# Optimization experiments

Hardware: AMD Instinct MI355X
Metric: run time of the kernel (lower is better)

Reference implementation:

```python
import jax, jax.numpy as jnp
import numpy as np

B, L, H, E, R = 2, 512, 768, 512, 32768
H2 = H // 2


def setup_inputs() -> dict:
    key = jax.random.key(0)
    ks = jax.random.split(key, 16)
    s = 0.02
    inp = {
        "hidden_states": jax.random.normal(ks[0], (B, L, H), dtype=jnp.float32),
        "ent_start": jax.random.randint(ks[1], (B, E), 0, L, dtype=jnp.int32),
        "ent_label": jax.random.randint(ks[2], (B, E), 0, 3, dtype=jnp.int32),
        "rel_head": jax.random.randint(ks[3], (B, R), 0, E, dtype=jnp.int32),
        "rel_tail": jax.random.randint(ks[4], (B, R), 0, E, dtype=jnp.int32),
        "rel_label": jax.random.randint(ks[5], (B, R), 0, 2, dtype=jnp.int32),
        "entity_emb": jax.random.normal(ks[6], (3, H), dtype=jnp.float32) * s,
        "head_W1": jax.random.normal(ks[7], (2 * H, H), dtype=jnp.float32) * s,
        "head_b1": jnp.zeros((H,), dtype=jnp.float32),
        "head_W2": jax.random.normal(ks[8], (H, H2), dtype=jnp.float32) * s,
        "head_b2": jnp.zeros((H2,), dtype=jnp.float32),
        "tail_W1": jax.random.normal(ks[9], (2 * H, H), dtype=jnp.float32) * s,
        "tail_b1": jnp.zeros((H,), dtype=jnp.float32),
        "tail_W2": jax.random.normal(ks[10], (H, H2), dtype=jnp.float32) * s,
        "tail_b2": jnp.zeros((H2,), dtype=jnp.float32),
        "bil_W": jax.random.normal(ks[11], (2, H2, H2), dtype=jnp.float32) * s,
        "lin_W": jax.random.normal(ks[12], (2 * H2, 2), dtype=jnp.float32) * s,
        "lin_b": jnp.zeros((2,), dtype=jnp.float32),
    }
    return inp


def _mlp(x, W1, b1, W2, b2):
    # Linear -> ReLU -> (dropout=identity) -> Linear -> ReLU -> (dropout=identity)
    h = jax.nn.relu(jnp.einsum("brd,dh->brh", x, W1) + b1)
    return jax.nn.relu(jnp.einsum("brh,hk->brk", h, W2) + b2)


def reference(hidden_states, ent_start, ent_label, rel_head, rel_tail, rel_label,
              entity_emb, head_W1, head_b1, head_W2, head_b2,
              tail_W1, tail_b1, tail_W2, tail_b2, bil_W, lin_W, lin_b):
    # Gather entity start token index and label for each relation endpoint
    h_idx = jnp.take_along_axis(ent_start, rel_head, axis=1)  # [B,R]
    t_idx = jnp.take_along_axis(ent_start, rel_tail, axis=1)
    h_lab = jnp.take_along_axis(ent_label, rel_head, axis=1)
    t_lab = jnp.take_along_axis(ent_label, rel_tail, axis=1)

    # Gather hidden states at entity start positions: [B,R,H]
    h_tok = jnp.take_along_axis(hidden_states, h_idx[..., None], axis=1)
    t_tok = jnp.take_along_axis(hidden_states, t_idx[..., None], axis=1)

    head_repr = jnp.concatenate([h_tok, entity_emb[h_lab]], axis=-1)  # [B,R,2H]
    tail_repr = jnp.concatenate([t_tok, entity_emb[t_lab]], axis=-1)

    heads = _mlp(head_repr, head_W1, head_b1, head_W2, head_b2)  # [B,R,H2]
    tails = _mlp(tail_repr, tail_W1, tail_b1, tail_W2, tail_b2)

    # BiaffineAttention: bilinear(x1,x2) + linear(cat(x1,x2))
    bil = jnp.einsum("brd,ode,bre->bro", heads, bil_W, tails)  # [B,R,2]
    lin = jnp.einsum("brc,co->bro", jnp.concatenate([heads, tails], axis=-1), lin_W) + lin_b
    logits = bil + lin  # [B,R,2]

    # Per-doc mean cross-entropy, summed over docs (matches loss accumulation)
    logp = jax.nn.log_softmax(logits, axis=-1)
    ce = -jnp.take_along_axis(logp, rel_label[..., None], axis=-1)[..., 0]  # [B,R]
    loss = ce.mean(axis=-1).sum()

    return loss, logits.reshape(B * R, 2)
```

## Files before the change

kernel.cpp:

```cpp
#include <hip/hip_runtime.h>
#include <math.h>

#define BB 2
#define LL 512
#define HH 768
#define EE 512
#define RR 32768
#define H2 384
#define MM 1024

typedef __attribute__((ext_vector_type(8))) short     bf16x8;
typedef __attribute__((ext_vector_type(4))) float     f32x4;
typedef __attribute__((ext_vector_type(8))) unsigned short u16x8;

#define BUFE (64 * 136)

__device__ __forceinline__ unsigned short f2bf(float f) {
    unsigned int u = __float_as_uint(f);
    u = (u + 0x7FFFu + ((u >> 16) & 1u)) >> 16;
    return (unsigned short)u;
}

__device__ __forceinline__ void wtrans(const float* __restrict__ src,
                                       unsigned short* __restrict__ dst,
                                       int K, int N, int tile, unsigned short* T)
{
    const int t = threadIdx.x;
    const int tn = N >> 5;
    const int n0 = (tile % tn) * 32;
    const int k0 = (tile / tn) * 32;
    const int r  = t >> 3;
    const int c4 = (t & 7) * 4;
    const float4 g = *(const float4*)(src + (size_t)(k0 + r) * N + n0 + c4);
    T[(c4 + 0) * 40 + r] = f2bf(g.x);
    T[(c4 + 1) * 40 + r] = f2bf(g.y);
    T[(c4 + 2) * 40 + r] = f2bf(g.z);
    T[(c4 + 3) * 40 + r] = f2bf(g.w);
    __syncthreads();
    const int n  = t >> 3;
    const int k4 = (t & 7) * 4;
    *(ushort4*)(dst + (size_t)(n0 + n) * K + k0 + k4) = *(ushort4*)&T[n * 40 + k4];
}

__global__ __launch_bounds__(256) void prep(
    const float* __restrict__ hW1, const float* __restrict__ tW1,
    unsigned short* __restrict__ W1ht, unsigned short* __restrict__ W1tt,
    const float* __restrict__ hidden, const int* __restrict__ ent_start,
    const float* __restrict__ emb,
    const float* __restrict__ hb1, const float* __restrict__ tb1,
    unsigned short* __restrict__ Hbf, float* __restrict__ embc,
    float* __restrict__ hlin, float* __restrict__ tlin, float* __restrict__ out)
{
    __shared__ unsigned short T[32 * 40];
    __shared__ float red[4][192];
    const int bid = blockIdx.x;
    const int t = threadIdx.x;

    if (bid == 2200) {
        const float4 z = {0.f, 0.f, 0.f, 0.f};
        ((float4*)hlin)[t] = z; ((float4*)hlin)[256 + t] = z;
        ((float4*)tlin)[t] = z; ((float4*)tlin)[256 + t] = z;
        if (t == 0) out[0] = 0.f;
        return;
    }

    if (bid >= 2176) {
        const int eb = bid - 2176;
        const int tc = t & 63;
        const int kg = t >> 6;
        const int n = eb * 64 + tc;
        const float* W = (n < 768) ? hW1 : tW1;
        const int cc = (n < 768) ? n : n - 768;
        float a0 = 0.f, a1 = 0.f, a2 = 0.f;
        const int kbeg = kg * 192;
        #pragma unroll 8
        for (int k = kbeg; k < kbeg + 192; ++k) {
            const float w = W[(size_t)(768 + k) * 768 + cc];
            a0 += emb[k] * w;
            a1 += emb[768 + k] * w;
            a2 += emb[1536 + k] * w;
        }
        red[kg][0 * 64 + tc] = a0;
        red[kg][1 * 64 + tc] = a1;
        red[kg][2 * 64 + tc] = a2;
        __syncthreads();
        if (kg == 0) {
            const float b = (n < 768) ? hb1[n] : tb1[n - 768];
            #pragma unroll
            for (int l = 0; l < 3; ++l) {
                embc[l * 1536 + n] = b + red[0][l * 64 + tc] + red[1][l * 64 + tc]
                                       + red[2][l * 64 + tc] + red[3][l * 64 + tc];
            }
        }
        return;
    }

    if (bid >= 1152) {
        const int m = bid - 1152;
        if (t >= 96) return;
        const int b = m >> 9;
        const int idx = ent_start[m];
        const float4* s = (const float4*)(hidden + (size_t)(b * LL + idx) * HH);
        const float4 v0 = s[2 * t];
        const float4 v1 = s[2 * t + 1];
        u16x8 o;
        o[0] = f2bf(v0.x); o[1] = f2bf(v0.y); o[2] = f2bf(v0.z); o[3] = f2bf(v0.w);
        o[4] = f2bf(v1.x); o[5] = f2bf(v1.y); o[6] = f2bf(v1.z); o[7] = f2bf(v1.w);
        *(u16x8*)(Hbf + (size_t)m * 768 + 8 * t) = o;
        return;
    }

    if (bid < 576) wtrans(hW1, W1ht, 768, 768, bid, T);
    else           wtrans(tW1, W1tt, 768, 768, bid - 576, T);
}

template<bool RELU, bool BIAS, bool EB, bool WF32, bool WBF16, bool O2, bool LIN>
__device__ __forceinline__ void gemm_body(
    int tile, int nx,
    const unsigned short* __restrict__ A, int lda, int aoff1,
    const unsigned short* __restrict__ Bt0, const unsigned short* __restrict__ Bt1,
    int ldb, int bt_mrow, int Nh,
    const float* __restrict__ bias0, const float* __restrict__ bias1,
    const float* __restrict__ embc, const int* __restrict__ labels,
    const float* __restrict__ linW, float* __restrict__ hlin, float* __restrict__ tlin,
    int K, float* __restrict__ Cf, unsigned short* __restrict__ Cb, int ldc,
    unsigned short* As, unsigned short* Bs)
{
    const int tid = threadIdx.x;
    const int n0 = (tile % nx) * 64;
    const int m0 = (tile / nx) * 64;
    const int hf = (n0 >= Nh) ? 1 : 0;
    const unsigned short* Bt = hf ? Bt1 : Bt0;
    const int nc0 = n0 - (hf ? Nh : 0);
    const int aoff = hf ? aoff1 : 0;

    const int sr = tid >> 2;
    const int sk = (tid & 3) * 32;

    const unsigned short* Ap = A + (size_t)(m0 + sr) * lda + aoff + sk;
    const unsigned short* Bp = Bt + (size_t)((m0 >> 9) * bt_mrow + nc0 + sr) * ldb + sk;

    const int lane = tid & 63;
    const int wave = tid >> 6;
    const int wm = (wave & 1) * 32;
    const int wn = (wave >> 1) * 32;
    const int l15 = lane & 15;
    const int quad = lane >> 4;

    f32x4 acc00 = {}, acc01 = {}, acc10 = {}, acc11 = {};

    u16x8 av0 = *(const u16x8*)(Ap);      u16x8 av1 = *(const u16x8*)(Ap + 8);
    u16x8 av2 = *(const u16x8*)(Ap + 16); u16x8 av3 = *(const u16x8*)(Ap + 24);
    u16x8 bv0 = *(const u16x8*)(Bp);      u16x8 bv1 = *(const u16x8*)(Bp + 8);
    u16x8 bv2 = *(const u16x8*)(Bp + 16); u16x8 bv3 = *(const u16x8*)(Bp + 24);
    const int swo = sr * 136 + sk;
    *(u16x8*)&As[swo] = av0;      *(u16x8*)&As[swo + 8] = av1;
    *(u16x8*)&As[swo + 16] = av2; *(u16x8*)&As[swo + 24] = av3;
    *(u16x8*)&Bs[swo] = bv0;      *(u16x8*)&Bs[swo + 8] = bv1;
    *(u16x8*)&Bs[swo + 16] = bv2; *(u16x8*)&Bs[swo + 24] = bv3;

    const int NT = K >> 7;
    const int aro = quad * 8;
    int cur = 0;
    for (int it = 0; it < NT; ++it) {
        if (it + 1 < NT) {
            const int ko = (it + 1) * 128;
            av0 = *(const u16x8*)(Ap + ko);      av1 = *(const u16x8*)(Ap + ko + 8);
            av2 = *(const u16x8*)(Ap + ko + 16); av3 = *(const u16x8*)(Ap + ko + 24);
            bv0 = *(const u16x8*)(Bp + ko);      bv1 = *(const u16x8*)(Bp + ko + 8);
            bv2 = *(const u16x8*)(Bp + ko + 16); bv3 = *(const u16x8*)(Bp + ko + 24);
        }
        asm volatile("s_waitcnt lgkmcnt(0)" ::: "memory");
        __builtin_amdgcn_s_barrier();
        __builtin_amdgcn_sched_barrier(0);
        const unsigned short* Ac = As + cur * BUFE;
        const unsigned short* Bc = Bs + cur * BUFE;
        #pragma unroll
        for (int s = 0; s < 4; ++s) {
            const int ks = s * 32 + aro;
            const bf16x8 fa0 = *(const bf16x8*)&Ac[(wm + l15) * 136 + ks];
            const bf16x8 fa1 = *(const bf16x8*)&Ac[(wm + 16 + l15) * 136 + ks];
            const bf16x8 fb0 = *(const bf16x8*)&Bc[(wn + l15) * 136 + ks];
            const bf16x8 fb1 = *(const bf16x8*)&Bc[(wn + 16 + l15) * 136 + ks];
            acc00 = __builtin_amdgcn_mfma_f32_16x16x32_bf16(fa0, fb0, acc00, 0, 0, 0);
            acc01 = __builtin_amdgcn_mfma_f32_16x16x32_bf16(fa0, fb1, acc01, 0, 0, 0);
            acc10 = __builtin_amdgcn_mfma_f32_16x16x32_bf16(fa1, fb0, acc10, 0, 0, 0);
            acc11 = __builtin_amdgcn_mfma_f32_16x16x32_bf16(fa1, fb1, acc11, 0, 0, 0);
        }
        if (it + 1 < NT) {
            unsigned short* Aw = As + (cur ^ 1) * BUFE;
            unsigned short* Bw = Bs + (cur ^ 1) * BUFE;
            *(u16x8*)&Aw[swo] = av0;      *(u16x8*)&Aw[swo + 8] = av1;
            *(u16x8*)&Aw[swo + 16] = av2; *(u16x8*)&Aw[swo + 24] = av3;
            *(u16x8*)&Bw[swo] = bv0;      *(u16x8*)&Bw[swo + 8] = bv1;
            *(u16x8*)&Bw[swo + 16] = bv2; *(u16x8*)&Bw[swo + 24] = bv3;
        }
        cur ^= 1;
    }

    float bias_v0 = 0.f, bias_v1 = 0.f;
    if (BIAS) {
        const float* bb = hf ? bias1 : bias0;
        bias_v0 = bb[nc0 + wn + l15];
        bias_v1 = bb[nc0 + wn + 16 + l15];
    }
    const int col0 = n0 + wn + l15;
    const int col1 = col0 + 16;
    int colw0 = col0, colw1 = col1;
    if (O2) {
        colw0 = 2 * (nc0 + wn + l15) + hf;
        colw1 = 2 * (nc0 + wn + 16 + l15) + hf;
    }
    float2 lw0 = {0.f, 0.f}, lw1 = {0.f, 0.f};
    float* lout = nullptr;
    if (LIN) {
        lw0 = ((const float2*)linW)[col0];
        lw1 = ((const float2*)linW)[col1];
        lout = hf ? tlin : hlin;
    }
    const f32x4 accs[2][2] = {{acc00, acc01}, {acc10, acc11}};
    #pragma unroll
    for (int mi = 0; mi < 2; ++mi) {
        #pragma unroll
        for (int r = 0; r < 4; ++r) {
            const int row = m0 + wm + mi * 16 + quad * 4 + r;
            float v0 = accs[mi][0][r];
            float v1 = accs[mi][1][r];
            if (BIAS) { v0 += bias_v0; v1 += bias_v1; }
            if (EB) {
                const int lab = labels[row];
                v0 += embc[lab * 1536 + col0];
                v1 += embc[lab * 1536 + col1];
            }
            if (RELU) { v0 = fmaxf(v0, 0.f); v1 = fmaxf(v1, 0.f); }
            if (WF32) {
                Cf[(size_t)row * ldc + colw0] = v0;
                Cf[(size_t)row * ldc + colw1] = v1;
            }
            if (WBF16) {
                Cb[(size_t)row * ldc + colw0] = f2bf(v0);
                Cb[(size_t)row * ldc + colw1] = f2bf(v1);
            }
            if (LIN) {
                float s0 = v0 * lw0.x + v1 * lw1.x;
                float s1 = v0 * lw0.y + v1 * lw1.y;
                #pragma unroll
                for (int o = 8; o >= 1; o >>= 1) {
                    s0 += __shfl_xor(s0, o, 64);
                    s1 += __shfl_xor(s1, o, 64);
                }
                if (l15 == 0) {
                    atomicAdd(&lout[2 * row],     s0);
                    atomicAdd(&lout[2 * row + 1], s1);
                }
            }
        }
    }
}

template<bool RELU, bool BIAS, bool EB, bool WF32, bool WBF16, bool O2, bool LIN>
__global__ __launch_bounds__(256) void gemm_mfma(
    const unsigned short* __restrict__ A, int lda, int aoff1,
    const unsigned short* __restrict__ Bt0, const unsigned short* __restrict__ Bt1,
    int ldb, int bt_mrow, int Nh,
    const float* __restrict__ bias0, const float* __restrict__ bias1,
    const float* __restrict__ embc, const int* __restrict__ labels,
    const float* __restrict__ linW, float* __restrict__ hlin, float* __restrict__ tlin,
    int K, float* __restrict__ Cf, unsigned short* __restrict__ Cb, int ldc)
{
    __shared__ __align__(16) unsigned short As[2 * BUFE];
    __shared__ __align__(16) unsigned short Bs[2 * BUFE];
    gemm_body<RELU, BIAS, EB, WF32, WBF16, O2, LIN>(
        blockIdx.y * gridDim.x + blockIdx.x, gridDim.x,
        A, lda, aoff1, Bt0, Bt1, ldb, bt_mrow, Nh,
        bias0, bias1, embc, labels, linW, hlin, tlin,
        K, Cf, Cb, ldc, As, Bs);
}

__global__ __launch_bounds__(256) void gemm1_plus(
    const unsigned short* __restrict__ Hbf,
    const unsigned short* __restrict__ W1ht, const unsigned short* __restrict__ W1tt,
    const float* __restrict__ embc, const int* __restrict__ ent_label,
    unsigned short* __restrict__ Y1bf,
    const float* __restrict__ hW2, const float* __restrict__ tW2,
    const float* __restrict__ bilW,
    unsigned short* __restrict__ W2ht, unsigned short* __restrict__ W2tt,
    unsigned short* __restrict__ bW0t, unsigned short* __restrict__ bW1t)
{
    __shared__ __align__(16) unsigned short As[2 * BUFE];
    __shared__ __align__(16) unsigned short Bs[2 * BUFE];
    const int bid = blockIdx.x;
    if (bid >= 384) {
        const int task = bid - 384;
        if (task < 288)      wtrans(hW2, W2ht, 768, 384, task, As);
        else if (task < 576) wtrans(tW2, W2tt, 768, 384, task - 288, As);
        else if (task < 720) wtrans(bilW, bW0t, 384, 384, task - 576, As);
        else                 wtrans(bilW + 384 * 384, bW1t, 384, 384, task - 720, As);
        return;
    }
    gemm_body<true, false, true, false, true, false, false>(
        bid, 24, Hbf, 768, 0, W1ht, W1tt, 768, 0, 768,
        nullptr, nullptr, embc, ent_label, nullptr, nullptr, nullptr,
        768, nullptr, Y1bf, 1536, As, Bs);
}

__global__ __launch_bounds__(256) void rel_gather(
    const float* __restrict__ Stab,
    const float* __restrict__ hlin, const float* __restrict__ tlin,
    const float* __restrict__ lin_b,
    const int* __restrict__ rel_head, const int* __restrict__ rel_tail,
    const int* __restrict__ rel_label,
    float* __restrict__ out)
{
    const int tid = threadIdx.x;
    const int i = blockIdx.x * 256 + tid;
    const int b = i >> 15;
    const int h = rel_head[i];
    const int t = rel_tail[i];
    const int lab = rel_label[i];
    const int mh = (b << 9) + h;
    const int mt = (b << 9) + t;

    const float2 hl = ((const float2*)hlin)[mh];
    const float2 tl = ((const float2*)tlin)[mt];
    const float2 zz = *(const float2*)(Stab + (size_t)mh * 1024 + 2 * t);
    const float z0 = zz.x + hl.x + tl.x + lin_b[0];
    const float z1 = zz.y + hl.y + tl.y + lin_b[1];
    out[1 + 2 * (size_t)i] = z0;
    out[2 + 2 * (size_t)i] = z1;

    const float mx = fmaxf(z0, z1);
    const float mn = fminf(z0, z1);
    const float lse = mx + log1pf(expf(mn - mx));
    float ce = lse - (lab ? z1 : z0);

    #pragma unroll
    for (int o = 32; o >= 1; o >>= 1) ce += __shfl_xor(ce, o, 64);
    __shared__ float wsum[4];
    if ((tid & 63) == 0) wsum[tid >> 6] = ce;
    __syncthreads();
    if (tid == 0) {
        const float bs = wsum[0] + wsum[1] + wsum[2] + wsum[3];
        atomicAdd(out, bs * (1.0f / (float)RR));
    }
}

extern "C" void kernel_launch(void* const* d_in, const int* in_sizes, int n_in,
                              void* d_out, int out_size, void* d_ws, size_t ws_size,
                              hipStream_t stream) {
    const float* hidden    = (const float*)d_in[0];
    const int*   ent_start = (const int*)d_in[1];
    const int*   ent_label = (const int*)d_in[2];
    const int*   rel_head  = (const int*)d_in[3];
    const int*   rel_tail  = (const int*)d_in[4];
    const int*   rel_label = (const int*)d_in[5];
    const float* emb       = (const float*)d_in[6];
    const float* head_W1   = (const float*)d_in[7];
    const float* head_b1   = (const float*)d_in[8];
    const float* head_W2   = (const float*)d_in[9];
    const float* head_b2   = (const float*)d_in[10];
    const float* tail_W1   = (const float*)d_in[11];
    const float* tail_b1   = (const float*)d_in[12];
    const float* tail_W2   = (const float*)d_in[13];
    const float* tail_b2   = (const float*)d_in[14];
    const float* bil_W     = (const float*)d_in[15];
    const float* lin_W     = (const float*)d_in[16];
    const float* lin_b     = (const float*)d_in[17];
    float* out = (float*)d_out;

    char* w = (char*)d_ws;
    auto carve = [&](size_t bytes) {
        char* p = w; w += (bytes + 255) & ~(size_t)255; return p;
    };
    unsigned short* Hbf  = (unsigned short*)carve((size_t)MM * 768 * 2);
    unsigned short* Y1bf = (unsigned short*)carve((size_t)MM * 1536 * 2);
    unsigned short* HTbf = (unsigned short*)carve((size_t)MM * 768 * 2);
    unsigned short* hWbf = (unsigned short*)carve((size_t)MM * 768 * 2);
    float*          Stab = (float*)carve((size_t)MM * 1024 * 4);
    unsigned short* W1ht = (unsigned short*)carve((size_t)768 * 768 * 2);
    unsigned short* W1tt = (unsigned short*)carve((size_t)768 * 768 * 2);
    unsigned short* W2ht = (unsigned short*)carve((size_t)384 * 768 * 2);
    unsigned short* W2tt = (unsigned short*)carve((size_t)384 * 768 * 2);
    unsigned short* bW0t = (unsigned short*)carve((size_t)384 * 384 * 2);
    unsigned short* bW1t = (unsigned short*)carve((size_t)384 * 384 * 2);
    float*          embc = (float*)carve((size_t)3 * 1536 * 4);
    float*          hlin = (float*)carve(2048 * 4);
    float*          tlin = (float*)carve(2048 * 4);

    prep<<<2201, 256, 0, stream>>>(
        head_W1, tail_W1, W1ht, W1tt,
        hidden, ent_start, emb, head_b1, tail_b1, Hbf, embc,
        hlin, tlin, out);

    gemm1_plus<<<1248, 256, 0, stream>>>(
        Hbf, W1ht, W1tt, embc, ent_label, Y1bf,
        head_W2, tail_W2, bil_W, W2ht, W2tt, bW0t, bW1t);

    gemm_mfma<true, true, false, false, true, false, true>
        <<<dim3(12, 16), 256, 0, stream>>>(
        Y1bf, 1536, 768, W2ht, W2tt, 768, 0, 384, head_b2, tail_b2,
        nullptr, nullptr, lin_W, hlin, tlin, 768, nullptr, HTbf, 768);

    gemm_mfma<false, false, false, false, true, false, false>
        <<<dim3(12, 16), 256, 0, stream>>>(
        HTbf, 768, 0, bW0t, bW1t, 384, 0, 384, nullptr, nullptr,
        nullptr, nullptr, nullptr, nullptr, nullptr, 384, nullptr, hWbf, 768);

    gemm_mfma<false, false, false, true, false, true, false>
        <<<dim3(16, 16), 256, 0, stream>>>(
        hWbf, 768, 384, HTbf + 384, HTbf + 384, 768, 512, 512,
        nullptr, nullptr, nullptr, nullptr, nullptr, nullptr, nullptr,
        384, Stab, nullptr, 1024);

    rel_gather<<<256, 256, 0, stream>>>(Stab, hlin, tlin, lin_b,
                                        rel_head, rel_tail, rel_label, out);
}
```

Measured before the change: 147.4 us.

## Halve GEMM K-tile to 64 and prefetch two stages ahead in registers

The bf16 MFMA GEMM tile loop drops its K step from 128 to 64 and shrinks the LDS buffers to match. Global loads now go two register sets (P and Q) ahead, alternating between two LDS buffers, so more loads are in flight relative to compute. This uses less LDS per block, which may allow higher occupancy. The cost is twice as many barriers per unit of K, and NT must be even or the last tile is mishandled.

Result: faster. 143.1 us (-3.0%).

```diff
diff --git a/kernel.cpp b/kernel.cpp
--- a/kernel.cpp
+++ b/kernel.cpp
@@ -13,7 +13,7 @@
 typedef __attribute__((ext_vector_type(4))) float     f32x4;
 typedef __attribute__((ext_vector_type(8))) unsigned short u16x8;
 
-#define BUFE (64 * 136)
+#define BUFE (64 * 72)
 
 __device__ __forceinline__ unsigned short f2bf(float f) {
     unsigned int u = __float_as_uint(f);
@@ -135,7 +135,7 @@
     const int aoff = hf ? aoff1 : 0;
 
     const int sr = tid >> 2;
-    const int sk = (tid & 3) * 32;
+    const int sk = (tid & 3) * 16;
 
     const unsigned short* Ap = A + (size_t)(m0 + sr) * lda + aoff + sk;
     const unsigned short* Bp = Bt + (size_t)((m0 >> 9) * bt_mrow + nc0 + sr) * ldb + sk;
@@ -146,57 +146,69 @@
     const int wn = (wave >> 1) * 32;
     const int l15 = lane & 15;
     const int quad = lane >> 4;
+    const int swo = sr * 72 + sk;
+    const int aro = quad * 8;
 
     f32x4 acc00 = {}, acc01 = {}, acc10 = {}, acc11 = {};
 
-    u16x8 av0 = *(const u16x8*)(Ap);      u16x8 av1 = *(const u16x8*)(Ap + 8);
-    u16x8 av2 = *(const u16x8*)(Ap + 16); u16x8 av3 = *(const u16x8*)(Ap + 24);
-    u16x8 bv0 = *(const u16x8*)(Bp);      u16x8 bv1 = *(const u16x8*)(Bp + 8);
-    u16x8 bv2 = *(const u16x8*)(Bp + 16); u16x8 bv3 = *(const u16x8*)(Bp + 24);
-    const int swo = sr * 136 + sk;
-    *(u16x8*)&As[swo] = av0;      *(u16x8*)&As[swo + 8] = av1;
-    *(u16x8*)&As[swo + 16] = av2; *(u16x8*)&As[swo + 24] = av3;
-    *(u16x8*)&Bs[swo] = bv0;      *(u16x8*)&Bs[swo + 8] = bv1;
-    *(u16x8*)&Bs[swo + 16] = bv2; *(u16x8*)&Bs[swo + 24] = bv3;
-
-    const int NT = K >> 7;
-    const int aro = quad * 8;
-    int cur = 0;
-    for (int it = 0; it < NT; ++it) {
-        if (it + 1 < NT) {
-            const int ko = (it + 1) * 128;
-            av0 = *(const u16x8*)(Ap + ko);      av1 = *(const u16x8*)(Ap + ko + 8);
-            av2 = *(const u16x8*)(Ap + ko + 16); av3 = *(const u16x8*)(Ap + ko + 24);
-            bv0 = *(const u16x8*)(Bp + ko);      bv1 = *(const u16x8*)(Bp + ko + 8);
-            bv2 = *(const u16x8*)(Bp + ko + 16); bv3 = *(const u16x8*)(Bp + ko + 24);
-        }
-        asm volatile("s_waitcnt lgkmcnt(0)" ::: "memory");
-        __builtin_amdgcn_s_barrier();
-        __builtin_amdgcn_sched_barrier(0);
-        const unsigned short* Ac = As + cur * BUFE;
-        const unsigned short* Bc = Bs + cur * BUFE;
-        #pragma unroll
-        for (int s = 0; s < 4; ++s) {
-            const int ks = s * 32 + aro;
-            const bf16x8 fa0 = *(const bf16x8*)&Ac[(wm + l15) * 136 + ks];
-            const bf16x8 fa1 = *(const bf16x8*)&Ac[(wm + 16 + l15) * 136 + ks];
-            const bf16x8 fb0 = *(const bf16x8*)&Bc[(wn + l15) * 136 + ks];
-            const bf16x8 fb1 = *(const bf16x8*)&Bc[(wn + 16 + l15) * 136 + ks];
-            acc00 = __builtin_amdgcn_mfma_f32_16x16x32_bf16(fa0, fb0, acc00, 0, 0, 0);
-            acc01 = __builtin_amdgcn_mfma_f32_16x16x32_bf16(fa0, fb1, acc01, 0, 0, 0);
-            acc10 = __builtin_amdgcn_mfma_f32_16x16x32_bf16(fa1, fb0, acc10, 0, 0, 0);
-            acc11 = __builtin_amdgcn_mfma_f32_16x16x32_bf16(fa1, fb1, acc11, 0, 0, 0);
-        }
-        if (it + 1 < NT) {
-            unsigned short* Aw = As + (cur ^ 1) * BUFE;
-            unsigned short* Bw = Bs + (cur ^ 1) * BUFE;
-            *(u16x8*)&Aw[swo] = av0;      *(u16x8*)&Aw[swo + 8] = av1;
-            *(u16x8*)&Aw[swo + 16] = av2; *(u16x8*)&Aw[swo + 24] = av3;
-            *(u16x8*)&Bw[swo] = bv0;      *(u16x8*)&Bw[swo + 8] = bv1;
-            *(u16x8*)&Bw[swo + 16] = bv2; *(u16x8*)&Bw[swo + 24] = bv3;
-        }
-        cur ^= 1;
-    }
+    u16x8 pa0, pa1, pb0, pb1;
+    u16x8 qa0, qa1, qb0, qb1;
+
+#define GLOADP(ko) { pa0 = *(const u16x8*)(Ap + (ko)); pa1 = *(const u16x8*)(Ap + (ko) + 8); \
+                     pb0 = *(const u16x8*)(Bp + (ko)); pb1 = *(const u16x8*)(Bp + (ko) + 8); }
+#define GLOADQ(ko) { qa0 = *(const u16x8*)(Ap + (ko)); qa1 = *(const u16x8*)(Ap + (ko) + 8); \
+                     qb0 = *(const u16x8*)(Bp + (ko)); qb1 = *(const u16x8*)(Bp + (ko) + 8); }
+#define SWRITEP(bi) { unsigned short* Aw = As + (bi) * BUFE; unsigned short* Bw = Bs + (bi) * BUFE; \
+                      *(u16x8*)&Aw[swo] = pa0; *(u16x8*)&Aw[swo + 8] = pa1; \
+                      *(u16x8*)&Bw[swo] = pb0; *(u16x8*)&Bw[swo + 8] = pb1; }
+#define SWRITEQ(bi) { unsigned short* Aw = As + (bi) * BUFE; unsigned short* Bw = Bs + (bi) * BUFE; \
+                      *(u16x8*)&Aw[swo] = qa0; *(u16x8*)&Aw[swo + 8] = qa1; \
+                      *(u16x8*)&Bw[swo] = qb0; *(u16x8*)&Bw[swo + 8] = qb1; }
+#define BAR() { asm volatile("s_waitcnt lgkmcnt(0)" ::: "memory"); \
+                __builtin_amdgcn_s_barrier(); \
+                __builtin_amdgcn_sched_barrier(0); }
+#define MFMA8(bi) { const unsigned short* Ac = As + (bi) * BUFE; \
+                    const unsigned short* Bc = Bs + (bi) * BUFE; \
+        const bf16x8 fa0 = *(const bf16x8*)&Ac[(wm + l15) * 72 + aro]; \
+        const bf16x8 fa1 = *(const bf16x8*)&Ac[(wm + 16 + l15) * 72 + aro]; \
+        const bf16x8 fb0 = *(const bf16x8*)&Bc[(wn + l15) * 72 + aro]; \
+        const bf16x8 fb1 = *(const bf16x8*)&Bc[(wn + 16 + l15) * 72 + aro]; \
+        const bf16x8 ga0 = *(const bf16x8*)&Ac[(wm + l15) * 72 + aro + 32]; \
+        const bf16x8 ga1 = *(const bf16x8*)&Ac[(wm + 16 + l15) * 72 + aro + 32]; \
+        const bf16x8 gb0 = *(const bf16x8*)&Bc[(wn + l15) * 72 + aro + 32]; \
+        const bf16x8 gb1 = *(const bf16x8*)&Bc[(wn + 16 + l15) * 72 + aro + 32]; \
+        acc00 = __builtin_amdgcn_mfma_f32_16x16x32_bf16(fa0, fb0, acc00, 0, 0, 0); \
+        acc01 = __builtin_amdgcn_mfma_f32_16x16x32_bf16(fa0, fb1, acc01, 0, 0, 0); \
+        acc10 = __builtin_amdgcn_mfma_f32_16x16x32_bf16(fa1, fb0, acc10, 0, 0, 0); \
+        acc11 = __builtin_amdgcn_mfma_f32_16x16x32_bf16(fa1, fb1, acc11, 0, 0, 0); \
+        acc00 = __builtin_amdgcn_mfma_f32_16x16x32_bf16(ga0, gb0, acc00, 0, 0, 0); \
+        acc01 = __builtin_amdgcn_mfma_f32_16x16x32_bf16(ga0, gb1, acc01, 0, 0, 0); \
+        acc10 = __builtin_amdgcn_mfma_f32_16x16x32_bf16(ga1, gb0, acc10, 0, 0, 0); \
+        acc11 = __builtin_amdgcn_mfma_f32_16x16x32_bf16(ga1, gb1, acc11, 0, 0, 0); }
+
+    const int NT = K >> 6;
+
+    GLOADP(0);
+    GLOADQ(64);
+    SWRITEP(0);
+
+    for (int it = 0; it < NT; it += 2) {
+        BAR();
+        if (it + 2 < NT) GLOADP((it + 2) << 6);
+        MFMA8(0);
+        SWRITEQ(1);
+        BAR();
+        if (it + 3 < NT) GLOADQ((it + 3) << 6);
+        MFMA8(1);
+        if (it + 2 < NT) SWRITEP(0);
+    }
+
+#undef GLOADP
+#undef GLOADQ
+#undef SWRITEP
+#undef SWRITEQ
+#undef BAR
+#undef MFMA8
 
     float bias_v0 = 0.f, bias_v1 = 0.f;
     if (BIAS) {
```
